# Kernel optimization log

Hardware: AMD Instinct MI355X
Metric: run time of the kernel (lower is better)

The kernel has to match this reference:

```python
import jax, jax.numpy as jnp
import numpy as np

LAMBDA_L1, LAMBDA_IOU, LAMBDA_CLS = 5.0, 2.0, 1.0
B, N, K, M = 16, 900, 91, 100


def setup_inputs() -> dict:
    key = jax.random.key(0)
    k1, k2, k3, k4, k5, k6 = jax.random.split(key, 6)
    cls_pred = jax.random.normal(k1, (B, N, K), dtype=jnp.float32)
    # valid xyxy boxes in [0,1]
    pmin = jax.random.uniform(k2, (B, N, 2), dtype=jnp.float32) * 0.5
    pwh = jax.random.uniform(k3, (B, N, 2), dtype=jnp.float32) * 0.5 + 1e-3
    bb_pred = jnp.concatenate([pmin, pmin + pwh], axis=-1)
    gmin = jax.random.uniform(k4, (B, M, 2), dtype=jnp.float32) * 0.5
    gwh = jax.random.uniform(k5, (B, M, 2), dtype=jnp.float32) * 0.5 + 1e-3
    bb_gt = jnp.concatenate([gmin, gmin + gwh], axis=-1)
    cls_gt = jax.random.randint(k6, (B, M), 0, K)
    return {"cls_pred": cls_pred, "bb_pred": bb_pred, "cls_gt": cls_gt, "bb_gt": bb_gt}


def _box_iou(b1, b2):
    # b1 [P,4], b2 [Q,4] -> iou [P,Q]
    area1 = (b1[:, 2] - b1[:, 0]) * (b1[:, 3] - b1[:, 1])
    area2 = (b2[:, 2] - b2[:, 0]) * (b2[:, 3] - b2[:, 1])
    x_min = jnp.maximum(b1[:, None, 0], b2[None, :, 0])
    y_min = jnp.maximum(b1[:, None, 1], b2[None, :, 1])
    x_max = jnp.minimum(b1[:, None, 2], b2[None, :, 2])
    y_max = jnp.minimum(b1[:, None, 3], b2[None, :, 3])
    inter = jnp.clip(x_max - x_min, 0) * jnp.clip(y_max - y_min, 0)
    union = area1[:, None] + area2[None, :] - inter
    return inter / (union + 1e-6)


def _solve(cost):
    # Jonker-Volgenant shortest augmenting path; cost (n, m) with n <= m; minimization.
    n, m = cost.shape
    u = np.zeros(n + 1)
    v = np.zeros(m + 1)
    p = np.zeros(m + 1, dtype=np.int64)   # p[j] = row matched to col j (1-indexed)
    way = np.zeros(m + 1, dtype=np.int64)
    for i in range(1, n + 1):
        p[0] = i
        j0 = 0
        minv = np.full(m + 1, np.inf)
        used = np.zeros(m + 1, dtype=bool)
        while True:
            used[j0] = True
            i0 = p[j0]
            cur = cost[i0 - 1] - u[i0] - v[1:]
            cur = np.where(used[1:], np.inf, cur)
            upd = cur < minv[1:]
            minv[1:] = np.where(upd, cur, minv[1:])
            way[1:] = np.where(upd, j0, way[1:])
            cand = np.where(used[1:], np.inf, minv[1:])
            j1 = int(np.argmin(cand)) + 1
            delta = cand[j1 - 1]
            uj = np.nonzero(used)[0]
            u[p[uj]] += delta
            v[uj] -= delta
            minv[1:] = np.where(used[1:], minv[1:], minv[1:] - delta)
            j0 = j1
            if p[j0] == 0:
                break
        while j0 != 0:
            j1 = way[j0]
            p[j0] = p[j1]
            j0 = j1
    cols = np.nonzero(p[1:])[0]
    rows = p[1:][cols] - 1
    return rows, cols


def _linear_sum_assignment(cost):
    cost = np.asarray(cost, dtype=np.float64)
    transposed = cost.shape[0] > cost.shape[1]
    rows, cols = _solve(cost.T if transposed else cost)
    if transposed:
        rows, cols = cols, rows
    order = np.argsort(rows)
    return rows[order], cols[order]


def reference(cls_pred, bb_pred, cls_gt, bb_gt):
    b, n, k = cls_pred.shape
    m = cls_gt.shape[1]
    out_prob = jax.nn.softmax(cls_pred.reshape(b * n, k), axis=-1)
    out_bbox = bb_pred.reshape(b * n, 4)
    tgt_ids = cls_gt.reshape(-1)
    tgt_bbox = bb_gt.reshape(-1, 4)
    cost_class = -out_prob[:, tgt_ids]                                   # [B*N, B*M]
    l1 = jnp.sum(jnp.abs(out_bbox[:, None, :] - tgt_bbox[None, :, :]), -1)  # p=1 cdist
    iou = -_box_iou(out_bbox, tgt_bbox)
    C = LAMBDA_IOU * iou + LAMBDA_L1 * l1 + LAMBDA_CLS * cost_class
    C = np.asarray(C.reshape(b, n, b, m))
    Cb = C[np.arange(b), :, np.arange(b), :]  # diagonal blocks [B, N, M] (= torch split(sizes)[i][i])
    preds, tgts = [], []
    for bi in range(b):
        r, c = _linear_sum_assignment(Cb[bi])
        preds.append(r)
        tgts.append(c)
    return (jnp.asarray(np.stack(preds), dtype=jnp.int64),
            jnp.asarray(np.stack(tgts), dtype=jnp.int64))
```

## Files before the change

### kernel.cpp

```cpp
#include <hip/hip_runtime.h>
#include <math.h>

#define NB 16
#define NP 900
#define NC 91
#define NT 100
#define SLOTS 15

__global__ __launch_bounds__(256) void colcost_kernel(
    const float* __restrict__ cls_pred,
    const float* __restrict__ bb_pred,
    const int*   __restrict__ cls_gt,
    const float* __restrict__ bb_gt,
    float* __restrict__ Ct,
    unsigned* __restrict__ colOwner)
{
    const int b    = blockIdx.x;
    const int wid  = threadIdx.x >> 6;
    const int lane = threadIdx.x & 63;
    const int n0   = blockIdx.y * 4;
    const int n    = n0 + wid;

    __shared__ float probs[4][NC];
    __shared__ float sCt[NT][5];

    if (lane == 0) colOwner[(size_t)b*NP + n] = 0xFFFFFFFFu;

    const float* crow = cls_pred + ((size_t)b*NP + n)*NC;
    const float x0 = crow[lane];
    const float x1 = (lane + 64 < NC) ? crow[lane + 64] : -INFINITY;
    float mx = fmaxf(x0, x1);
    #pragma unroll
    for (int off = 32; off >= 1; off >>= 1)
        mx = fmaxf(mx, __shfl_xor(mx, off, 64));
    float s = expf(x0 - mx);
    if (lane + 64 < NC) s += expf(x1 - mx);
    #pragma unroll
    for (int off = 32; off >= 1; off >>= 1)
        s += __shfl_xor(s, off, 64);
    const float rinv = 1.0f / s;

    probs[wid][lane] = expf(x0 - mx) * rinv;
    if (lane + 64 < NC) probs[wid][lane + 64] = expf(x1 - mx) * rinv;
    __syncthreads();

    const float4 bp = *reinterpret_cast<const float4*>(bb_pred + ((size_t)b*NP + n)*4);
    const float parea = (bp.z - bp.x) * (bp.w - bp.y);

    #pragma unroll
    for (int h = 0; h < 2; ++h) {
        const int m = lane + 64*h;
        if (m < NT) {
            const int row = b*NT + m;
            const float4 gt = *reinterpret_cast<const float4*>(bb_gt + (size_t)row*4);
            const float garea = (gt.z - gt.x) * (gt.w - gt.y);
            const int   c     = cls_gt[row];

            const float l1 = fabsf(bp.x - gt.x) + fabsf(bp.y - gt.y) +
                             fabsf(bp.z - gt.z) + fabsf(bp.w - gt.w);
            const float xm = fmaxf(bp.x, gt.x);
            const float ym = fmaxf(bp.y, gt.y);
            const float xM = fminf(bp.z, gt.z);
            const float yM = fminf(bp.w, gt.w);
            const float inter = fmaxf(xM - xm, 0.f) * fmaxf(yM - ym, 0.f);
            const float iou = inter / (parea + garea - inter + 1e-6f);
            const float pc  = probs[wid][c];

            sCt[m][wid] = 5.0f*l1 - 2.0f*iou - pc;
        }
    }
    __syncthreads();

    for (int t = threadIdx.x; t < NT*4; t += 256) {
        const int m = t >> 2, c = t & 3;
        Ct[(size_t)(b*NT + m)*NP + n0 + c] = sCt[m][c];
    }
}

__global__ __launch_bounds__(256) void rowmin_claim_kernel(
    const float* __restrict__ Ct,
    float* __restrict__ u_init,
    int*   __restrict__ amin,
    unsigned* __restrict__ colOwner)
{
    const int b    = blockIdx.x;
    const int wid  = threadIdx.x >> 6;
    const int lane = threadIdx.x & 63;
    const int m    = blockIdx.y * 4 + wid;
    const int row  = b*NT + m;
    const float* cr = Ct + (size_t)row * NP;

    float best = INFINITY; int bj = 0;
    #pragma unroll
    for (int r = 0; r < SLOTS; ++r) {
        const int j = 64*r + lane;
        if ((r < SLOTS-1) || (lane < 4)) {
            const float x = cr[j];
            if (x < best) { best = x; bj = j; }
        }
    }
    float vmin = best;
    #pragma unroll
    for (int off = 32; off >= 1; off >>= 1)
        vmin = fminf(vmin, __shfl_xor(vmin, off, 64));
    const unsigned long long win = __ballot(best == vmin);
    const int bjAll = __shfl(bj, __builtin_ctzll(win), 64);
    if (lane == 0) {
        u_init[row] = vmin;
        amin[row]   = bjAll;
        atomicMin(&colOwner[(size_t)b*NP + bjAll], (unsigned)m);
    }
}

__device__ __forceinline__ int pop_row(unsigned long long& fm0, unsigned long long& fm1)
{
    if (fm0) { const int l = __builtin_ctzll(fm0); fm0 &= fm0 - 1; return l + 1;  }
    if (fm1) { const int l = __builtin_ctzll(fm1); fm1 &= fm1 - 1; return l + 65; }
    return 0;
}

__global__ __launch_bounds__(64) void jv_kernel(
    const float* __restrict__ Ct,
    const float* __restrict__ u_init,
    const int*   __restrict__ amin,
    const unsigned* __restrict__ colOwner,
    int* __restrict__ out)
{
    const int b    = blockIdx.x;
    const int lane = threadIdx.x;
    const float* Cb = Ct + (size_t)b*NT*NP;

    double v[SLOTS], minv[SLOTS];
    float  cw[SLOTS], cnext[SLOTS];
    int    way[SLOTS], p[SLOTS];

    double u0 = (double)u_init[b*NT + lane];
    double u1 = (lane < NT-64) ? (double)u_init[b*NT + 64 + lane] : 0.0;

    #pragma unroll
    for (int r = 0; r < SLOTS; ++r) {
        v[r] = 0.0; way[r] = 0;
        unsigned o = 0xFFFFFFFFu;
        if ((r < SLOTS-1) || (lane < 4)) o = colOwner[(size_t)b*NP + 64*r + lane];
        p[r] = (o == 0xFFFFFFFFu) ? 0 : (int)o + 1;
    }

    const int a0 = amin[b*NT + lane];
    const bool as0 = (colOwner[(size_t)b*NP + a0] == (unsigned)lane);
    bool as1 = true;
    if (lane < NT-64) {
        const int a1 = amin[b*NT + 64 + lane];
        as1 = (colOwner[(size_t)b*NP + a1] == (unsigned)(64 + lane));
    }
    unsigned long long fm0 = __ballot(!as0);
    unsigned long long fm1 = __ballot(!as1 && (lane < NT-64));

    int iCur = pop_row(fm0, fm1);
    if (iCur) {
        const float* cr = Cb + (size_t)(iCur-1)*NP;
        #pragma unroll
        for (int r = 0; r < SLOTS; ++r) {
            int ja = 64*r + lane; if (ja > NP-1) ja = NP-1;
            cnext[r] = cr[ja];
        }
    }

    while (iCur) {
        const int iNext = pop_row(fm0, fm1);

        unsigned usedMask = 0;
        bool it0 = false, it1 = false;
        double Dtot = 0.0;
        #pragma unroll
        for (int r = 0; r < SLOTS; ++r) { minv[r] = INFINITY; cw[r] = cnext[r]; }

        const int i = iCur;
        if (i <= 64) { if (lane == i-1)  it0 = true; }
        else         { if (lane == i-65) it1 = true; }
        double ui0 = (i <= 64) ? __shfl(u0, i-1, 64) : __shfl(u1, i-65, 64);

        if (iNext) {
            const float* cr = Cb + (size_t)(iNext-1)*NP;
            #pragma unroll
            for (int r = 0; r < SLOTS; ++r) {
                int ja = 64*r + lane; if (ja > NP-1) ja = NP-1;
                cnext[r] = cr[ja];
            }
        }

        int j0 = 0, jfinal;
        while (true) {
            double best = INFINITY;
            int    pk   = 0;
            #pragma unroll
            for (int r = 0; r < SLOTS; ++r) {
                const int jm1 = 64*r + lane;
                const bool valid = ((r < SLOTS-1) || (lane < 4)) && !((usedMask >> r) & 1u);
                const double cur = valid ? (((double)cw[r] - ui0) - v[r]) : INFINITY;
                if (cur < minv[r]) { minv[r] = cur; way[r] = j0; }
                if (minv[r] < best) { best = minv[r]; pk = (jm1 + 1) | (p[r] << 10); }
            }

            const float bf = (float)best;
            float vm32 = bf;
            #pragma unroll
            for (int off = 32; off >= 1; off >>= 1)
                vm32 = fminf(vm32, __shfl_xor(vm32, off, 64));
            const unsigned long long cand = __ballot(bf <= vm32 + 1e-3f);
            int winner;
            if (__popcll(cand) == 1) {
                winner = __builtin_ctzll(cand);
            } else {
                double vm = best;
                #pragma unroll
                for (int off = 32; off >= 1; off >>= 1)
                    vm = fmin(vm, __shfl_xor(vm, off, 64));
                winner = __builtin_ctzll(__ballot(best == vm));
            }
            const double delta = __shfl(best, winner, 64);
            pk = __shfl(pk, winner, 64);

            const int j1    = pk & 1023;
            const int pnext = pk >> 10;
            Dtot += delta;
            #pragma unroll
            for (int r = 0; r < SLOTS; ++r) minv[r] -= delta;

            #pragma unroll
            for (int r = 0; r < SLOTS; ++r) {
                if (64*r + lane + 1 == j1) {
                    usedMask |= 1u << r;
                    minv[r] = INFINITY;
                    v[r] += Dtot;
                }
            }

            if (pnext == 0) { jfinal = j1; break; }

            ui0 = (pnext <= 64) ? __shfl(u0, pnext-1, 64) : __shfl(u1, pnext-65, 64);
            if (pnext <= 64) { if (lane == pnext-1)  { u0 -= Dtot; it0 = true; } }
            else             { if (lane == pnext-65) { u1 -= Dtot; it1 = true; } }

            {
                const float* cr = Cb + (size_t)(pnext-1)*NP;
                #pragma unroll
                for (int r = 0; r < SLOTS; ++r) {
                    int ja = 64*r + lane; if (ja > NP-1) ja = NP-1;
                    cw[r] = cr[ja];
                }
            }
            j0 = j1;
        }

        {
            int jc = jfinal;
            while (jc != 0) {
                int wsel = 0;
                #pragma unroll
                for (int r = 0; r < SLOTS; ++r)
                    if (64*r + lane + 1 == jc) wsel = way[r];
                const int jprev = __shfl(wsel, (jc-1) & 63, 64);
                int newrow;
                if (jprev == 0) newrow = i;
                else {
                    int psel = 0;
                    #pragma unroll
                    for (int r = 0; r < SLOTS; ++r)
                        if (64*r + lane + 1 == jprev) psel = p[r];
                    newrow = __shfl(psel, (jprev-1) & 63, 64);
                }
                #pragma unroll
                for (int r = 0; r < SLOTS; ++r)
                    if (64*r + lane + 1 == jc) p[r] = newrow;
                jc = jprev;
            }
        }

        #pragma unroll
        for (int r = 0; r < SLOTS; ++r)
            if ((usedMask >> r) & 1u) v[r] -= Dtot;
        if (it0) u0 += Dtot;
        if (it1) u1 += Dtot;

        iCur = iNext;
    }

    int base = 0;
    #pragma unroll
    for (int r = 0; r < SLOTS; ++r) {
        const unsigned long long mask = __ballot(p[r] != 0);
        if (p[r] != 0) {
            const int rank = base + (int)__popcll(mask & ((1ull << lane) - 1ull));
            out[b*NT + rank]         = 64*r + lane;
            out[NB*NT + b*NT + rank] = p[r] - 1;
        }
        base += (int)__popcll(mask);
    }
}

extern "C" void kernel_launch(void* const* d_in, const int* in_sizes, int n_in,
                              void* d_out, int out_size, void* d_ws, size_t ws_size,
                              hipStream_t stream)
{
    const float* cls_pred = (const float*)d_in[0];
    const float* bb_pred  = (const float*)d_in[1];
    const int*   cls_gt   = (const int*)d_in[2];
    const float* bb_gt    = (const float*)d_in[3];

    char* base = (char*)d_ws;
    const size_t ctBytes = (size_t)NB*NT*NP*sizeof(float);
    float*    Ct       = (float*)base;
    unsigned* colOwner = (unsigned*)(base + ctBytes);
    float*    u_init   = (float*)(base + ctBytes + (size_t)NB*NP*4);
    int*      aminP    = (int*)(base + ctBytes + (size_t)NB*NP*4 + (size_t)NB*NT*4);

    colcost_kernel<<<dim3(NB, NP/4), 256, 0, stream>>>(
        cls_pred, bb_pred, cls_gt, bb_gt, Ct, colOwner);
    rowmin_claim_kernel<<<dim3(NB, NT/4), 256, 0, stream>>>(Ct, u_init, aminP, colOwner);
    jv_kernel<<<NB, 64, 0, stream>>>(Ct, u_init, aminP, colOwner, (int*)d_out);
}
```

Measured before the change: 45.27 us.

## Fuse row-min claim step into JV kernel using shared-memory column owners

Removes the separate row-minimum/claim kernel and performs it inside the JV kernel, with 4 waves per batch block computing row minima and claiming columns through shared-memory atomics. Column owner, u_init and argmin now live in LDS, so the global colOwner initialization and the workspace round trips go away. This saves one kernel launch and some global traffic. In exchange, only 16 blocks now do the row-min pass instead of 400, and the JV block carries three idle waves.

```diff
diff --git a/kernel.cpp b/kernel.cpp
--- a/kernel.cpp
+++ b/kernel.cpp
@@ -12,8 +12,7 @@
     const float* __restrict__ bb_pred,
     const int*   __restrict__ cls_gt,
     const float* __restrict__ bb_gt,
-    float* __restrict__ Ct,
-    unsigned* __restrict__ colOwner)
+    float* __restrict__ Ct)
 {
     const int b    = blockIdx.x;
     const int wid  = threadIdx.x >> 6;
@@ -23,8 +22,6 @@
 
     __shared__ float probs[4][NC];
     __shared__ float sCt[NT][5];
-
-    if (lane == 0) colOwner[(size_t)b*NP + n] = 0xFFFFFFFFu;
 
     const float* crow = cls_pred + ((size_t)b*NP + n)*NC;
     const float x0 = crow[lane];
@@ -77,41 +74,6 @@
     }
 }
 
-__global__ __launch_bounds__(256) void rowmin_claim_kernel(
-    const float* __restrict__ Ct,
-    float* __restrict__ u_init,
-    int*   __restrict__ amin,
-    unsigned* __restrict__ colOwner)
-{
-    const int b    = blockIdx.x;
-    const int wid  = threadIdx.x >> 6;
-    const int lane = threadIdx.x & 63;
-    const int m    = blockIdx.y * 4 + wid;
-    const int row  = b*NT + m;
-    const float* cr = Ct + (size_t)row * NP;
-
-    float best = INFINITY; int bj = 0;
-    #pragma unroll
-    for (int r = 0; r < SLOTS; ++r) {
-        const int j = 64*r + lane;
-        if ((r < SLOTS-1) || (lane < 4)) {
-            const float x = cr[j];
-            if (x < best) { best = x; bj = j; }
-        }
-    }
-    float vmin = best;
-    #pragma unroll
-    for (int off = 32; off >= 1; off >>= 1)
-        vmin = fminf(vmin, __shfl_xor(vmin, off, 64));
-    const unsigned long long win = __ballot(best == vmin);
-    const int bjAll = __shfl(bj, __builtin_ctzll(win), 64);
-    if (lane == 0) {
-        u_init[row] = vmin;
-        amin[row]   = bjAll;
-        atomicMin(&colOwner[(size_t)b*NP + bjAll], (unsigned)m);
-    }
-}
-
 __device__ __forceinline__ int pop_row(unsigned long long& fm0, unsigned long long& fm1)
 {
     if (fm0) { const int l = __builtin_ctzll(fm0); fm0 &= fm0 - 1; return l + 1;  }
@@ -119,38 +81,71 @@
     return 0;
 }
 
-__global__ __launch_bounds__(64) void jv_kernel(
+__global__ __launch_bounds__(256) void jv_kernel(
     const float* __restrict__ Ct,
-    const float* __restrict__ u_init,
-    const int*   __restrict__ amin,
-    const unsigned* __restrict__ colOwner,
     int* __restrict__ out)
 {
     const int b    = blockIdx.x;
-    const int lane = threadIdx.x;
+    const int tid  = threadIdx.x;
+    const int wid  = tid >> 6;
+    const int lane = tid & 63;
     const float* Cb = Ct + (size_t)b*NT*NP;
+
+    __shared__ int   sOwner[NP];
+    __shared__ float sU[NT];
+    __shared__ int   sAmin[NT];
+
+    for (int j = tid; j < NP; j += 256) sOwner[j] = 0x7FFFFFFF;
+    __syncthreads();
+
+    for (int m = wid; m < NT; m += 4) {
+        const float* cr = Cb + (size_t)m * NP;
+        float best = INFINITY; int bj = 0;
+        #pragma unroll
+        for (int r = 0; r < SLOTS; ++r) {
+            const int j = 64*r + lane;
+            if ((r < SLOTS-1) || (lane < 4)) {
+                const float x = cr[j];
+                if (x < best) { best = x; bj = j; }
+            }
+        }
+        float vmin = best;
+        #pragma unroll
+        for (int off = 32; off >= 1; off >>= 1)
+            vmin = fminf(vmin, __shfl_xor(vmin, off, 64));
+        const unsigned long long win = __ballot(best == vmin);
+        const int bjAll = __shfl(bj, __builtin_ctzll(win), 64);
+        if (lane == 0) {
+            sU[m]    = vmin;
+            sAmin[m] = bjAll;
+            atomicMin(&sOwner[bjAll], m);
+        }
+    }
+    __syncthreads();
+
+    if (wid != 0) return;
 
     double v[SLOTS], minv[SLOTS];
     float  cw[SLOTS], cnext[SLOTS];
     int    way[SLOTS], p[SLOTS];
 
-    double u0 = (double)u_init[b*NT + lane];
-    double u1 = (lane < NT-64) ? (double)u_init[b*NT + 64 + lane] : 0.0;
+    double u0 = (double)sU[lane];
+    double u1 = (lane < NT-64) ? (double)sU[64 + lane] : 0.0;
 
     #pragma unroll
     for (int r = 0; r < SLOTS; ++r) {
         v[r] = 0.0; way[r] = 0;
-        unsigned o = 0xFFFFFFFFu;
-        if ((r < SLOTS-1) || (lane < 4)) o = colOwner[(size_t)b*NP + 64*r + lane];
-        p[r] = (o == 0xFFFFFFFFu) ? 0 : (int)o + 1;
-    }
-
-    const int a0 = amin[b*NT + lane];
-    const bool as0 = (colOwner[(size_t)b*NP + a0] == (unsigned)lane);
+        int o = 0x7FFFFFFF;
+        if ((r < SLOTS-1) || (lane < 4)) o = sOwner[64*r + lane];
+        p[r] = (o == 0x7FFFFFFF) ? 0 : o + 1;
+    }
+
+    const int a0 = sAmin[lane];
+    const bool as0 = (sOwner[a0] == lane);
     bool as1 = true;
     if (lane < NT-64) {
-        const int a1 = amin[b*NT + 64 + lane];
-        as1 = (colOwner[(size_t)b*NP + a1] == (unsigned)(64 + lane));
+        const int a1 = sAmin[64 + lane];
+        as1 = (sOwner[a1] == 64 + lane);
     }
     unsigned long long fm0 = __ballot(!as0);
     unsigned long long fm1 = __ballot(!as1 && (lane < NT-64));
@@ -307,15 +302,9 @@
     const int*   cls_gt   = (const int*)d_in[2];
     const float* bb_gt    = (const float*)d_in[3];
 
-    char* base = (char*)d_ws;
-    const size_t ctBytes = (size_t)NB*NT*NP*sizeof(float);
-    float*    Ct       = (float*)base;
-    unsigned* colOwner = (unsigned*)(base + ctBytes);
-    float*    u_init   = (float*)(base + ctBytes + (size_t)NB*NP*4);
-    int*      aminP    = (int*)(base + ctBytes + (size_t)NB*NP*4 + (size_t)NB*NT*4);
+    float* Ct = (float*)d_ws;
 
     colcost_kernel<<<dim3(NB, NP/4), 256, 0, stream>>>(
-        cls_pred, bb_pred, cls_gt, bb_gt, Ct, colOwner);
-    rowmin_claim_kernel<<<dim3(NB, NT/4), 256, 0, stream>>>(Ct, u_init, aminP, colOwner);
-    jv_kernel<<<NB, 64, 0, stream>>>(Ct, u_init, aminP, colOwner, (int*)d_out);
+        cls_pred, bb_pred, cls_gt, bb_gt, Ct);
+    jv_kernel<<<NB, 256, 0, stream>>>(Ct, (int*)d_out);
 }
```

After: 56.90 us. 25.7% more time.
